# Kernel optimization log

Hardware: AMD Instinct MI355X
Metric: run time of the kernel (lower is better)

The kernel has to match this reference:

```python
import jax, jax.numpy as jnp
import numpy as np

HEADS = 8
DIM_HEAD = 64
NUM_MEM_KV = 4
DIM = 512
B, H, W = 16, 32, 32


def setup_inputs() -> dict:
    key = jax.random.key(0)
    k1, k2, k3, k4 = jax.random.split(key, 4)
    hidden = HEADS * DIM_HEAD
    x = jax.random.normal(k1, (B, DIM, H, W), dtype=jnp.float32)
    gamma = jnp.zeros((DIM,), dtype=jnp.float32)  # nn.Parameter init zeros
    mem_kv = jax.random.normal(k2, (2, HEADS, NUM_MEM_KV, DIM_HEAD), dtype=jnp.float32)
    w_qkv = jax.random.normal(k3, (3 * hidden, DIM), dtype=jnp.float32) * (1.0 / np.sqrt(DIM))
    w_out = jax.random.normal(k4, (DIM, hidden), dtype=jnp.float32) * (1.0 / np.sqrt(hidden))
    return {"x": x, "gamma": gamma, "mem_kv": mem_kv, "w_qkv": w_qkv, "w_out": w_out}


def reference(x, gamma, mem_kv, w_qkv, w_out):
    b, c, h, w = x.shape
    n = h * w
    # RMSNorm: F.normalize over channel dim, then * (gamma+1) * sqrt(dim)
    denom = jnp.maximum(jnp.linalg.norm(x, axis=1, keepdims=True), 1e-12)
    xn = (x / denom) * (gamma[None, :, None, None] + 1.0) * (c ** 0.5)
    # 1x1 conv qkv projection
    qkv = jnp.einsum('bchw,oc->bohw', xn, w_qkv)  # [b, 3*hidden, h, w]
    q, k, v = jnp.split(qkv, 3, axis=1)

    def to_heads(t):
        # 'b (h c) x y -> b h (x y) c'
        return t.reshape(b, HEADS, DIM_HEAD, n).transpose(0, 1, 3, 2)

    q = to_heads(q) * (DIM_HEAD ** -0.5)  # [b, heads, n, d]
    k = to_heads(k)
    v = to_heads(v)
    mk = jnp.broadcast_to(mem_kv[0], (b, HEADS, NUM_MEM_KV, DIM_HEAD))
    mv = jnp.broadcast_to(mem_kv[1], (b, HEADS, NUM_MEM_KV, DIM_HEAD))
    k = jnp.concatenate([mk, k], axis=2)  # [b, heads, m+n, d]
    v = jnp.concatenate([mv, v], axis=2)
    sim = jnp.einsum('bhid,bhjd->bhij', q, k)
    attn = jax.nn.softmax(sim, axis=-1)
    out = jnp.einsum('bhij,bhjd->bhid', attn, v)  # [b, heads, n, d]
    # 'b h (x y) d -> b (h d) x y'
    out = out.transpose(0, 1, 3, 2).reshape(b, HEADS * DIM_HEAD, h, w)
    return jnp.einsum('bchw,oc->bohw', out, w_out)
```

## Files before the change

kernel.cpp:

```cpp
#include <hip/hip_runtime.h>
#include <cstdint>
#include <cstddef>

constexpr int kHeads = 8;
constexpr int kDHead = 64;
constexpr int kC     = 512;
constexpr int kB     = 16;
constexpr int kN     = 1024;
constexpr int kHid   = 512;

typedef _Float16 h16;
typedef _Float16 h8 __attribute__((ext_vector_type(8)));
typedef _Float16 h4 __attribute__((ext_vector_type(4)));
typedef _Float16 h2 __attribute__((ext_vector_type(2)));
typedef float f32x4 __attribute__((ext_vector_type(4)));

__global__ __launch_bounds__(256) void rms_transpose_kernel(
    const float* __restrict__ x, h16* __restrict__ xh)
{
  __shared__ float T[64 * 64];
  __shared__ float red[4][64];
  __shared__ float sl[64];
  const int t  = threadIdx.x;
  const int b  = blockIdx.x >> 4;
  const int p0 = (blockIdx.x & 15) << 6;
  const float* xb = x + (size_t)b * kC * kN + p0;

  const int pix = t & 63, sub = t >> 6;
  float sum = 0.f;
  #pragma unroll 8
  for (int c = sub * 128; c < sub * 128 + 128; ++c) {
    const float v = xb[(size_t)c * kN + pix];
    sum = fmaf(v, v, sum);
  }
  red[sub][pix] = sum;
  __syncthreads();
  if (t < 64) {
    const float tot = red[0][t] + red[1][t] + red[2][t] + red[3][t];
    sl[t] = 22.62741699796952f / fmaxf(sqrtf(tot), 1e-12f);
  }
  __syncthreads();

  for (int cc = 0; cc < 8; cc++) {
    const int c0 = cc * 64;
    #pragma unroll
    for (int i = 0; i < 4; i++) {
      const int r  = i * 16 + (t >> 4);
      const int pg = t & 15;
      const float4 v = *(const float4*)(xb + (size_t)(c0 + r) * kN + pg * 4);
      *(float4*)&T[r * 64 + ((pg ^ (r & 15)) << 2)] = v;
    }
    __syncthreads();
    #pragma unroll
    for (int i2 = 0; i2 < 2; i2++) {
      const int p  = i2 * 32 + (t >> 3);
      const int cg = t & 7;
      const float sc = sl[p];
      h16 hv[8];
      #pragma unroll
      for (int j = 0; j < 8; j++) {
        const int c = cg * 8 + j;
        const float v = T[c * 64 + (((p >> 2) ^ (c & 15)) << 2) + (p & 3)];
        hv[j] = (h16)(v * sc);
      }
      *(h8*)&xh[((size_t)b * kN + p0 + p) * kC + c0 + cg * 8] = *(h8*)hv;
    }
    __syncthreads();
  }
}

__global__ __launch_bounds__(64) void prep_w_kernel(
    const float* __restrict__ w_qkv, const float* __restrict__ gamma,
    const float* __restrict__ w_out, h16* __restrict__ wqh,
    h16* __restrict__ wouth)
{
  const int row = blockIdx.x;
  const int c0  = threadIdx.x * 8;
  if (row < 1536) {
    const float sc = (row < 512) ? 0.125f * 1.4426950408889634f : 1.f;
    const float4 a  = *(const float4*)(w_qkv + (size_t)row * kC + c0);
    const float4 b  = *(const float4*)(w_qkv + (size_t)row * kC + c0 + 4);
    const float4 g0 = *(const float4*)(gamma + c0);
    const float4 g1 = *(const float4*)(gamma + c0 + 4);
    h8 hv = { (h16)(a.x * (g0.x + 1.f) * sc), (h16)(a.y * (g0.y + 1.f) * sc),
              (h16)(a.z * (g0.z + 1.f) * sc), (h16)(a.w * (g0.w + 1.f) * sc),
              (h16)(b.x * (g1.x + 1.f) * sc), (h16)(b.y * (g1.y + 1.f) * sc),
              (h16)(b.z * (g1.z + 1.f) * sc), (h16)(b.w * (g1.w + 1.f) * sc) };
    *(h8*)&wqh[(size_t)row * kC + c0] = hv;
  } else {
    const int r = row - 1536;
    const float4 a = *(const float4*)(w_out + (size_t)r * kC + c0);
    const float4 b = *(const float4*)(w_out + (size_t)r * kC + c0 + 4);
    h8 hv = { (h16)a.x, (h16)a.y, (h16)a.z, (h16)a.w,
              (h16)b.x, (h16)b.y, (h16)b.z, (h16)b.w };
    *(h8*)&wouth[(size_t)r * kC + c0] = hv;
  }
}

__device__ __forceinline__ void gemm_loop_f16(
    const h16* __restrict__ Ag, const h16* __restrict__ Bg,
    h16 (*__restrict__ As)[8192], h16 (*__restrict__ Bs)[8192],
    int t, int w, int g, int lo, f32x4 (&acc)[4][4])
{
  const int wo = (w >> 1) * 64, wp = (w & 1) * 64;
  h8 stA[4], stB[4];
  auto load = [&](int kt) {
    const int k0 = kt * 64;
    #pragma unroll
    for (int i = 0; i < 4; i++) {
      const int f = t + i * 256, r = f >> 3, cg = f & 7;
      stA[i] = *(const h8*)(Ag + (size_t)r * kC + k0 + cg * 8);
      stB[i] = *(const h8*)(Bg + (size_t)r * kC + k0 + cg * 8);
    }
  };
  auto store = [&](int buf) {
    #pragma unroll
    for (int i = 0; i < 4; i++) {
      const int f = t + i * 256, r = f >> 3, cg = f & 7;
      const int off = r * 64 + ((cg ^ (r & 7)) << 3);
      *(h8*)&As[buf][off] = stA[i];
      *(h8*)&Bs[buf][off] = stB[i];
    }
  };
  load(0); store(0); __syncthreads();
  int buf = 0;
  for (int kt = 0; kt < 8; kt++) {
    if (kt < 7) load(kt + 1);
    h8 bfr[4][2];
    #pragma unroll
    for (int ni = 0; ni < 4; ni++) {
      const int row = wp + ni * 16 + lo;
      #pragma unroll
      for (int kb = 0; kb < 2; kb++)
        bfr[ni][kb] = *(const h8*)&Bs[buf][row * 64 + (((kb * 4 + g) ^ (row & 7)) << 3)];
    }
    #pragma unroll
    for (int mi = 0; mi < 4; mi++) {
      const int row = wo + mi * 16 + lo;
      const h8 a0 = *(const h8*)&As[buf][row * 64 + (((    g) ^ (row & 7)) << 3)];
      const h8 a1 = *(const h8*)&As[buf][row * 64 + (((4 + g) ^ (row & 7)) << 3)];
      #pragma unroll
      for (int ni = 0; ni < 4; ni++) {
        acc[mi][ni] = __builtin_amdgcn_mfma_f32_16x16x32_f16(a0, bfr[ni][0], acc[mi][ni], 0, 0, 0);
        acc[mi][ni] = __builtin_amdgcn_mfma_f32_16x16x32_f16(a1, bfr[ni][1], acc[mi][ni], 0, 0, 0);
      }
    }
    if (kt < 7) store(buf ^ 1);
    __syncthreads();
    buf ^= 1;
  }
}

__global__ __launch_bounds__(256) void qkv_mfma_kernel(
    const h16* __restrict__ xh, const h16* __restrict__ wqh,
    h16* __restrict__ Qh, h16* __restrict__ Kh, h16* __restrict__ VTh)
{
  __shared__ h16 As[2][8192];
  __shared__ h16 Bs[2][8192];
  const int t = threadIdx.x, lane = t & 63, w = t >> 6, g = lane >> 4, lo = lane & 15;
  const int o0 = blockIdx.x * 128;
  const int p0 = blockIdx.y * 128;
  const int b  = blockIdx.z;
  const h16* Ag = wqh + (size_t)o0 * kC;
  const h16* Bg = xh + ((size_t)b * kN + p0) * kC;

  f32x4 acc[4][4];
  #pragma unroll
  for (int mi = 0; mi < 4; mi++)
    #pragma unroll
    for (int ni = 0; ni < 4; ni++) { f32x4 z = {0.f, 0.f, 0.f, 0.f}; acc[mi][ni] = z; }

  gemm_loop_f16(Ag, Bg, As, Bs, t, w, g, lo, acc);

  const int o_wave = o0 + (w >> 1) * 64;
  const int which  = o_wave >> 9;
  const int head   = (o_wave >> 6) & 7;
  const size_t bh  = (size_t)b * kHeads + head;
  const int pglob  = p0 + (w & 1) * 64;

  if (which == 2) {
    h16* Vdst = VTh + bh * (size_t)(kN * kDHead);
    #pragma unroll
    for (int mi = 0; mi < 4; mi++)
      #pragma unroll
      for (int ni = 0; ni < 4; ni++) {
        const int p = pglob + ni * 16 + lo;
        #pragma unroll
        for (int r = 0; r < 4; r++) {
          const int d = mi * 16 + g * 4 + r;
          Vdst[(size_t)d * kN + p] = (h16)((const float*)&acc[mi][ni])[r];
        }
      }
  } else {
    h16* lw = &As[0][0] + w * 4096;
    #pragma unroll
    for (int mi = 0; mi < 4; mi++) {
      const int gran0 = mi * 2 + (g >> 1);
      const int off   = (g & 1) * 4;
      #pragma unroll
      for (int ni = 0; ni < 4; ni++) {
        const int p = ni * 16 + lo;
        h4 pv = { (h16)acc[mi][ni].x, (h16)acc[mi][ni].y,
                  (h16)acc[mi][ni].z, (h16)acc[mi][ni].w };
        *(h4*)&lw[p * 64 + ((gran0 ^ (p & 7)) << 3) + off] = pv;
      }
    }
    __syncthreads();
    h16* dst = (which ? Kh : Qh) + bh * (size_t)(kN * kDHead);
    #pragma unroll
    for (int i = 0; i < 8; i++) {
      const int p  = i * 8 + (lane >> 3);
      const int dg = lane & 7;
      const h8 v = *(const h8*)&lw[p * 64 + ((dg ^ (p & 7)) << 3)];
      *(h8*)&dst[((size_t)pglob + p) * kDHead + dg * 8] = v;
    }
  }
}

__global__ __launch_bounds__(256, 3) void attn_mfma_kernel(
    const h16* __restrict__ Qh, const h16* __restrict__ Kh,
    const h16* __restrict__ VTh, const float* __restrict__ mem_kv,
    h16* __restrict__ ah)
{
  __shared__ h16 Kl[2][4096];
  __shared__ h16 Vl[2][4096];

  const int t    = threadIdx.x;
  const int lane = t & 63;
  const int w    = t >> 6;
  const int g    = lane >> 4;
  const int lo   = lane & 15;
  const int id   = blockIdx.x;
  const int xcd  = id & 7;
  const int slot = id >> 3;
  const int grp  = xcd * 16 + (slot & 15);
  const int qt   = slot >> 4;
  const int h = grp & 7, b = grp >> 3;
  const size_t bh = (size_t)b * kHeads + h;

  const h16* Qg = Qh  + bh * 65536;
  const h16* Kg = Kh  + bh * 65536;
  const h16* Vg = VTh + bh * 65536;
  const int q0 = qt * 128 + w * 32;

  h8 qf[2][2];
  #pragma unroll
  for (int ni = 0; ni < 2; ni++)
    #pragma unroll
    for (int kb = 0; kb < 2; kb++)
      qf[ni][kb] = *(const h8*)(Qg + (size_t)(q0 + ni*16 + lo) * 64 + kb*32 + g*8);

  {
    const int kr = t >> 2, dq = (t & 3) << 4;
    h16 hv[16];
    if (kr < 4) {
      const float* src = mem_kv + (size_t)h * 256 + kr * 64 + dq;
      #pragma unroll
      for (int i = 0; i < 16; i++) hv[i] = (h16)src[i];
    } else {
      #pragma unroll
      for (int i = 0; i < 16; i++) hv[i] = (h16)0.f;
    }
    const int sw = (kr & 7) << 3;
    *(h8*)&Kl[0][kr*64 + ( dq      ^ sw)] = *(h8*)&hv[0];
    *(h8*)&Kl[0][kr*64 + ((dq + 8) ^ sw)] = *(h8*)&hv[8];

    const int d = t >> 2, kq = (t & 3) << 4;
    h16 vv[16];
    #pragma unroll
    for (int i = 0; i < 16; i++) vv[i] = (h16)0.f;
    if (kq == 0) {
      const float* src = mem_kv + 2048 + (size_t)h * 256 + d;
      #pragma unroll
      for (int i = 0; i < 4; i++) vv[i] = (h16)src[i * 64];
    }
    const int sv = (d & 7) << 3;
    *(h8*)&Vl[0][d*64 + ( kq      ^ sv)] = *(h8*)&vv[0];
    *(h8*)&Vl[0][d*64 + ((kq + 8) ^ sv)] = *(h8*)&vv[8];
  }
  __syncthreads();

  f32x4 o[2][4];
  #pragma unroll
  for (int qb = 0; qb < 2; qb++)
    #pragma unroll
    for (int db = 0; db < 4; db++) { f32x4 z = {0.f,0.f,0.f,0.f}; o[qb][db] = z; }
  float lst[2] = {0.f, 0.f};

  h8 stK[2], stV[2];

  auto proc = [&](const h16* KL, const h16* VL, h16* KW, h16* VW,
                  int loadIdx, bool mask) {
    if (loadIdx < 16) {
      const size_t key0 = (size_t)loadIdx * 64;
      #pragma unroll
      for (int ps = 0; ps < 2; ps++) {
        const int f = t + ps*256, r = f >> 3, cb = (f & 7) << 3;
        stK[ps] = *(const h8*)(Kg + (key0 + r) * 64 + cb);
        stV[ps] = *(const h8*)(Vg + (size_t)r * 1024 + key0 + cb);
      }
    }

    f32x4 s[4][2];
    __builtin_amdgcn_s_setprio(1);
    #pragma unroll
    for (int mi = 0; mi < 4; mi++) {
      const int row = mi*16 + lo;
      const int sw = (row & 7) << 3;
      const h8 k0 = *(const h8*)&KL[row*64 + (( g*8)      ^ sw)];
      const h8 k1 = *(const h8*)&KL[row*64 + ((32 + g*8)  ^ sw)];
      float ci = -8.f;
      if (mask && (mi > 0 || g > 0)) ci = -1e30f;
      const f32x4 cinit = {ci, ci, ci, ci};
      #pragma unroll
      for (int ni = 0; ni < 2; ni++) {
        f32x4 acc = __builtin_amdgcn_mfma_f32_16x16x32_f16(k0, qf[ni][0], cinit, 0, 0, 0);
        acc = __builtin_amdgcn_mfma_f32_16x16x32_f16(k1, qf[ni][1], acc, 0, 0, 0);
        s[mi][ni] = acc;
      }
    }
    __builtin_amdgcn_s_setprio(0);

    h4 p4[4][2];
    #pragma unroll
    for (int ni = 0; ni < 2; ni++) {
      #pragma unroll
      for (int mi = 0; mi < 4; mi++) {
        const float px = exp2f(s[mi][ni].x);
        const float py = exp2f(s[mi][ni].y);
        const float pz = exp2f(s[mi][ni].z);
        const float pw = exp2f(s[mi][ni].w);
        lst[ni] += (px + py) + (pz + pw);
        const h2 a = __builtin_bit_cast(h2, __builtin_amdgcn_cvt_pkrtz(px, py));
        const h2 c = __builtin_bit_cast(h2, __builtin_amdgcn_cvt_pkrtz(pz, pw));
        p4[mi][ni] = __builtin_shufflevector(a, c, 0, 1, 2, 3);
      }
    }

    __builtin_amdgcn_s_setprio(1);
    #pragma unroll
    for (int db = 0; db < 4; db++) {
      const int d = db*16 + lo;
      const int sw = (d & 7) << 3;
      h4 v4[4];
      #pragma unroll
      for (int mi = 0; mi < 4; mi++)
        v4[mi] = *(const h4*)&VL[d*64 + ((mi*16 + (g>>1)*8) ^ sw) + (g&1)*4];
      #pragma unroll
      for (int qb = 0; qb < 2; qb++)
        #pragma unroll
        for (int mi = 0; mi < 4; mi++)
          o[qb][db] = __builtin_amdgcn_mfma_f32_16x16x16f16(p4[mi][qb], v4[mi], o[qb][db], 0, 0, 0);
    }
    __builtin_amdgcn_s_setprio(0);

    if (loadIdx < 16) {
      #pragma unroll
      for (int ps = 0; ps < 2; ps++) {
        const int f = t + ps*256, r = f >> 3, cb = (f & 7) << 3;
        const int sw = (r & 7) << 3;
        *(h8*)&KW[r*64 + (cb ^ sw)] = stK[ps];
        *(h8*)&VW[r*64 + (cb ^ sw)] = stV[ps];
      }
    }
    __syncthreads();
  };

  proc(Kl[0], Vl[0], Kl[1], Vl[1], 0, true);
  #pragma unroll 1
  for (int i = 0; i < 8; i++) {
    proc(Kl[1], Vl[1], Kl[0], Vl[0], 2*i + 1, false);
    proc(Kl[0], Vl[0], Kl[1], Vl[1], 2*i + 2, false);
  }

  #pragma unroll
  for (int qb = 0; qb < 2; qb++) {
    float l = lst[qb];
    l += __shfl_xor(l, 16);
    l += __shfl_xor(l, 32);
    const float il = 1.f / l;
    const float i0 = __shfl(il, g*4 + 0);
    const float i1 = __shfl(il, g*4 + 1);
    const float i2 = __shfl(il, g*4 + 2);
    const float i3 = __shfl(il, g*4 + 3);
    const int qg = (b << 10) + q0 + qb*16 + g*4;
    #pragma unroll
    for (int db = 0; db < 4; db++) {
      const int c = h*64 + db*16 + lo;
      ah[(size_t)(qg + 0) * kHid + c] = (h16)(o[qb][db].x * i0);
      ah[(size_t)(qg + 1) * kHid + c] = (h16)(o[qb][db].y * i1);
      ah[(size_t)(qg + 2) * kHid + c] = (h16)(o[qb][db].z * i2);
      ah[(size_t)(qg + 3) * kHid + c] = (h16)(o[qb][db].w * i3);
    }
  }
}

__global__ __launch_bounds__(256) void out_mfma_kernel(
    const h16* __restrict__ ah, const h16* __restrict__ wouth,
    float* __restrict__ out)
{
  __shared__ h16 As[2][8192];
  __shared__ h16 Bs[2][8192];
  const int t = threadIdx.x, lane = t & 63, w = t >> 6, g = lane >> 4, lo = lane & 15;
  const int o0 = blockIdx.x * 128;
  const int p0 = blockIdx.y * 128;
  const int b  = blockIdx.z;
  const h16* Ag = wouth + (size_t)o0 * kC;
  const h16* Bg = ah + ((size_t)b * kN + p0) * kC;

  f32x4 acc[4][4];
  #pragma unroll
  for (int mi = 0; mi < 4; mi++)
    #pragma unroll
    for (int ni = 0; ni < 4; ni++) { f32x4 z = {0.f, 0.f, 0.f, 0.f}; acc[mi][ni] = z; }

  gemm_loop_f16(Ag, Bg, As, Bs, t, w, g, lo, acc);

  const int ow = o0 + (w >> 1) * 64;
  const int pw = p0 + (w & 1) * 64;
  #pragma unroll
  for (int mi = 0; mi < 4; mi++)
    #pragma unroll
    for (int ni = 0; ni < 4; ni++) {
      const int p = pw + ni * 16 + lo;
      #pragma unroll
      for (int r = 0; r < 4; r++) {
        const int oc = ow + mi * 16 + g * 4 + r;
        out[((size_t)b * kHid + oc) * kN + p] = ((const float*)&acc[mi][ni])[r];
      }
    }
}

extern "C" void kernel_launch(void* const* d_in, const int* in_sizes, int n_in,
                              void* d_out, int out_size, void* d_ws, size_t ws_size,
                              hipStream_t stream) {
  (void)in_sizes; (void)n_in; (void)out_size; (void)ws_size;
  const float* x      = (const float*)d_in[0];
  const float* gamma  = (const float*)d_in[1];
  const float* mem_kv = (const float*)d_in[2];
  const float* w_qkv  = (const float*)d_in[3];
  const float* w_out  = (const float*)d_in[4];
  float* out = (float*)d_out;

  h16* xh    = (h16*)d_ws;
  h16* Qh    = xh + (size_t)16777216;
  h16* Kh    = Qh + (size_t)8388608;
  h16* VTh   = Kh + (size_t)8388608;
  h16* ah    = VTh + (size_t)8388608;
  h16* wqh   = ah + (size_t)8388608;
  h16* wouth = wqh + (size_t)786432;

  rms_transpose_kernel<<<256, 256, 0, stream>>>(x, xh);
  prep_w_kernel<<<2048, 64, 0, stream>>>(w_qkv, gamma, w_out, wqh, wouth);
  qkv_mfma_kernel<<<dim3(12, 8, 16), 256, 0, stream>>>(xh, wqh, Qh, Kh, VTh);
  attn_mfma_kernel<<<1024, 256, 0, stream>>>(Qh, Kh, VTh, mem_kv, ah);
  out_mfma_kernel<<<dim3(4, 8, 16), 256, 0, stream>>>(ah, wouth, out);
}
```

Baseline: 154.8 us.

## Use single-wave attention blocks reading K/V from global with prepended memory-KV tile

Memory K/V is written once by a new prep kernel as a padded 64-key tile at the front of enlarged K and V^T buffers, and the QKV GEMM writes after that tile. The attention kernel becomes one wave per block, 4096 blocks, and loads K and V fragments straight from global memory instead of staging them in double-buffered, swizzled LDS with barriers. The padded zero keys are no longer masked; their fixed exp2(-8) contribution is subtracted from the softmax denominator. This removes LDS traffic and barriers, but each wave now waits on uncoalesced global/L2 loads with no prefetch, and K/V is re-read once per wave rather than once per block.

```diff
diff --git a/kernel.cpp b/kernel.cpp
--- a/kernel.cpp
+++ b/kernel.cpp
@@ -8,6 +8,8 @@
 constexpr int kB     = 16;
 constexpr int kN     = 1024;
 constexpr int kHid   = 512;
+constexpr int kKeys  = 1088;
+constexpr int kKVsz  = kKeys * kDHead;
 
 typedef _Float16 h16;
 typedef _Float16 h8 __attribute__((ext_vector_type(8)));
@@ -97,6 +99,33 @@
   }
 }
 
+__global__ __launch_bounds__(64) void prep_memkv_kernel(
+    const float* __restrict__ mem_kv, h16* __restrict__ Kh2,
+    h16* __restrict__ VT2)
+{
+  const int bh = blockIdx.x;
+  const int h  = bh & 7;
+  const int t  = threadIdx.x;
+  h16* krow = Kh2 + (size_t)bh * kKVsz + t * kDHead;
+  if (t < 4) {
+    const float* src = mem_kv + (size_t)h * 256 + t * 64;
+    #pragma unroll
+    for (int j = 0; j < 64; j++) krow[j] = (h16)src[j];
+  } else {
+    #pragma unroll
+    for (int j = 0; j < 8; j++) *(h8*)&krow[j * 8] = (h8)0;
+  }
+  h16* vrow = VT2 + (size_t)bh * kKVsz + (size_t)t * kKeys;
+  h16 tmp[64];
+  #pragma unroll
+  for (int j = 0; j < 64; j++) tmp[j] = (h16)0.f;
+  #pragma unroll
+  for (int k = 0; k < 4; k++)
+    tmp[k] = (h16)mem_kv[2048 + (size_t)h * 256 + k * 64 + t];
+  #pragma unroll
+  for (int j = 0; j < 8; j++) *(h8*)&vrow[j * 8] = *(h8*)&tmp[j * 8];
+}
+
 __device__ __forceinline__ void gemm_loop_f16(
     const h16* __restrict__ Ag, const h16* __restrict__ Bg,
     h16 (*__restrict__ As)[8192], h16 (*__restrict__ Bs)[8192],
@@ -153,7 +182,7 @@
 
 __global__ __launch_bounds__(256) void qkv_mfma_kernel(
     const h16* __restrict__ xh, const h16* __restrict__ wqh,
-    h16* __restrict__ Qh, h16* __restrict__ Kh, h16* __restrict__ VTh)
+    h16* __restrict__ Qh, h16* __restrict__ Kh2, h16* __restrict__ VT2)
 {
   __shared__ h16 As[2][8192];
   __shared__ h16 Bs[2][8192];
@@ -179,7 +208,7 @@
   const int pglob  = p0 + (w & 1) * 64;
 
   if (which == 2) {
-    h16* Vdst = VTh + bh * (size_t)(kN * kDHead);
+    h16* Vdst = VT2 + bh * kKVsz;
     #pragma unroll
     for (int mi = 0; mi < 4; mi++)
       #pragma unroll
@@ -188,7 +217,7 @@
         #pragma unroll
         for (int r = 0; r < 4; r++) {
           const int d = mi * 16 + g * 4 + r;
-          Vdst[(size_t)d * kN + p] = (h16)((const float*)&acc[mi][ni])[r];
+          Vdst[(size_t)d * kKeys + 64 + p] = (h16)((const float*)&acc[mi][ni])[r];
         }
       }
   } else {
@@ -206,7 +235,7 @@
       }
     }
     __syncthreads();
-    h16* dst = (which ? Kh : Qh) + bh * (size_t)(kN * kDHead);
+    h16* dst = which ? (Kh2 + bh * kKVsz + 64 * kDHead) : (Qh + bh * (size_t)(kN * kDHead));
     #pragma unroll
     for (int i = 0; i < 8; i++) {
       const int p  = i * 8 + (lane >> 3);
@@ -217,31 +246,24 @@
   }
 }
 
-__global__ __launch_bounds__(256, 3) void attn_mfma_kernel(
-    const h16* __restrict__ Qh, const h16* __restrict__ Kh,
-    const h16* __restrict__ VTh, const float* __restrict__ mem_kv,
-    h16* __restrict__ ah)
-{
-  __shared__ h16 Kl[2][4096];
-  __shared__ h16 Vl[2][4096];
-
-  const int t    = threadIdx.x;
-  const int lane = t & 63;
-  const int w    = t >> 6;
-  const int g    = lane >> 4;
-  const int lo   = lane & 15;
+__global__ __launch_bounds__(64, 3) void attn_mfma_kernel(
+    const h16* __restrict__ Qh, const h16* __restrict__ Kh2,
+    const h16* __restrict__ VT2, h16* __restrict__ ah)
+{
+  const int lane = threadIdx.x;
+  const int g  = lane >> 4;
+  const int lo = lane & 15;
   const int id   = blockIdx.x;
   const int xcd  = id & 7;
   const int slot = id >> 3;
   const int grp  = xcd * 16 + (slot & 15);
   const int qt   = slot >> 4;
   const int h = grp & 7, b = grp >> 3;
-  const size_t bh = (size_t)b * kHeads + h;
-
-  const h16* Qg = Qh  + bh * 65536;
-  const h16* Kg = Kh  + bh * 65536;
-  const h16* Vg = VTh + bh * 65536;
-  const int q0 = qt * 128 + w * 32;
+  const int q0 = qt * 32;
+
+  const h16* Qg = Qh  + (size_t)grp * (kN * kDHead);
+  const h16* Kg = Kh2 + (size_t)grp * kKVsz;
+  const h16* Vg = VT2 + (size_t)grp * kKVsz;
 
   h8 qf[2][2];
   #pragma unroll
@@ -250,68 +272,25 @@
     for (int kb = 0; kb < 2; kb++)
       qf[ni][kb] = *(const h8*)(Qg + (size_t)(q0 + ni*16 + lo) * 64 + kb*32 + g*8);
 
-  {
-    const int kr = t >> 2, dq = (t & 3) << 4;
-    h16 hv[16];
-    if (kr < 4) {
-      const float* src = mem_kv + (size_t)h * 256 + kr * 64 + dq;
-      #pragma unroll
-      for (int i = 0; i < 16; i++) hv[i] = (h16)src[i];
-    } else {
-      #pragma unroll
-      for (int i = 0; i < 16; i++) hv[i] = (h16)0.f;
-    }
-    const int sw = (kr & 7) << 3;
-    *(h8*)&Kl[0][kr*64 + ( dq      ^ sw)] = *(h8*)&hv[0];
-    *(h8*)&Kl[0][kr*64 + ((dq + 8) ^ sw)] = *(h8*)&hv[8];
-
-    const int d = t >> 2, kq = (t & 3) << 4;
-    h16 vv[16];
-    #pragma unroll
-    for (int i = 0; i < 16; i++) vv[i] = (h16)0.f;
-    if (kq == 0) {
-      const float* src = mem_kv + 2048 + (size_t)h * 256 + d;
-      #pragma unroll
-      for (int i = 0; i < 4; i++) vv[i] = (h16)src[i * 64];
-    }
-    const int sv = (d & 7) << 3;
-    *(h8*)&Vl[0][d*64 + ( kq      ^ sv)] = *(h8*)&vv[0];
-    *(h8*)&Vl[0][d*64 + ((kq + 8) ^ sv)] = *(h8*)&vv[8];
-  }
-  __syncthreads();
-
   f32x4 o[2][4];
   #pragma unroll
   for (int qb = 0; qb < 2; qb++)
     #pragma unroll
     for (int db = 0; db < 4; db++) { f32x4 z = {0.f,0.f,0.f,0.f}; o[qb][db] = z; }
   float lst[2] = {0.f, 0.f};
-
-  h8 stK[2], stV[2];
-
-  auto proc = [&](const h16* KL, const h16* VL, h16* KW, h16* VW,
-                  int loadIdx, bool mask) {
-    if (loadIdx < 16) {
-      const size_t key0 = (size_t)loadIdx * 64;
-      #pragma unroll
-      for (int ps = 0; ps < 2; ps++) {
-        const int f = t + ps*256, r = f >> 3, cb = (f & 7) << 3;
-        stK[ps] = *(const h8*)(Kg + (key0 + r) * 64 + cb);
-        stV[ps] = *(const h8*)(Vg + (size_t)r * 1024 + key0 + cb);
-      }
-    }
+  const f32x4 cinit = {-8.f, -8.f, -8.f, -8.f};
+
+  for (int kt = 0; kt < 17; kt++) {
+    const h16* Kt = Kg + kt * (64 * kDHead);
+    const int key0 = kt * 64;
 
     f32x4 s[4][2];
     __builtin_amdgcn_s_setprio(1);
     #pragma unroll
     for (int mi = 0; mi < 4; mi++) {
       const int row = mi*16 + lo;
-      const int sw = (row & 7) << 3;
-      const h8 k0 = *(const h8*)&KL[row*64 + (( g*8)      ^ sw)];
-      const h8 k1 = *(const h8*)&KL[row*64 + ((32 + g*8)  ^ sw)];
-      float ci = -8.f;
-      if (mask && (mi > 0 || g > 0)) ci = -1e30f;
-      const f32x4 cinit = {ci, ci, ci, ci};
+      const h8 k0 = *(const h8*)(Kt + row*64      + g*8);
+      const h8 k1 = *(const h8*)(Kt + row*64 + 32 + g*8);
       #pragma unroll
       for (int ni = 0; ni < 2; ni++) {
         f32x4 acc = __builtin_amdgcn_mfma_f32_16x16x32_f16(k0, qf[ni][0], cinit, 0, 0, 0);
@@ -341,11 +320,10 @@
     #pragma unroll
     for (int db = 0; db < 4; db++) {
       const int d = db*16 + lo;
-      const int sw = (d & 7) << 3;
       h4 v4[4];
       #pragma unroll
       for (int mi = 0; mi < 4; mi++)
-        v4[mi] = *(const h4*)&VL[d*64 + ((mi*16 + (g>>1)*8) ^ sw) + (g&1)*4];
+        v4[mi] = *(const h4*)(Vg + (size_t)d * kKeys + key0 + mi*16 + g*4);
       #pragma unroll
       for (int qb = 0; qb < 2; qb++)
         #pragma unroll
@@ -353,24 +331,6 @@
           o[qb][db] = __builtin_amdgcn_mfma_f32_16x16x16f16(p4[mi][qb], v4[mi], o[qb][db], 0, 0, 0);
     }
     __builtin_amdgcn_s_setprio(0);
-
-    if (loadIdx < 16) {
-      #pragma unroll
-      for (int ps = 0; ps < 2; ps++) {
-        const int f = t + ps*256, r = f >> 3, cb = (f & 7) << 3;
-        const int sw = (r & 7) << 3;
-        *(h8*)&KW[r*64 + (cb ^ sw)] = stK[ps];
-        *(h8*)&VW[r*64 + (cb ^ sw)] = stV[ps];
-      }
-    }
-    __syncthreads();
-  };
-
-  proc(Kl[0], Vl[0], Kl[1], Vl[1], 0, true);
-  #pragma unroll 1
-  for (int i = 0; i < 8; i++) {
-    proc(Kl[1], Vl[1], Kl[0], Vl[0], 2*i + 1, false);
-    proc(Kl[0], Vl[0], Kl[1], Vl[1], 2*i + 2, false);
   }
 
   #pragma unroll
@@ -378,6 +338,7 @@
     float l = lst[qb];
     l += __shfl_xor(l, 16);
     l += __shfl_xor(l, 32);
+    l -= 0.234375f;
     const float il = 1.f / l;
     const float i0 = __shfl(il, g*4 + 0);
     const float i1 = __shfl(il, g*4 + 1);
@@ -443,16 +404,17 @@
   float* out = (float*)d_out;
 
   h16* xh    = (h16*)d_ws;
-  h16* Qh    = xh + (size_t)16777216;
-  h16* Kh    = Qh + (size_t)8388608;
-  h16* VTh   = Kh + (size_t)8388608;
-  h16* ah    = VTh + (size_t)8388608;
-  h16* wqh   = ah + (size_t)8388608;
-  h16* wouth = wqh + (size_t)786432;
+  h16* Qh    = xh   + (size_t)16777216;
+  h16* Kh2   = Qh   + (size_t)8388608;
+  h16* VT2   = Kh2  + (size_t)8912896;
+  h16* ah    = VT2  + (size_t)8912896;
+  h16* wqh   = ah   + (size_t)8388608;
+  h16* wouth = wqh  + (size_t)786432;
 
   rms_transpose_kernel<<<256, 256, 0, stream>>>(x, xh);
   prep_w_kernel<<<2048, 64, 0, stream>>>(w_qkv, gamma, w_out, wqh, wouth);
-  qkv_mfma_kernel<<<dim3(12, 8, 16), 256, 0, stream>>>(xh, wqh, Qh, Kh, VTh);
-  attn_mfma_kernel<<<1024, 256, 0, stream>>>(Qh, Kh, VTh, mem_kv, ah);
+  prep_memkv_kernel<<<128, 64, 0, stream>>>(mem_kv, Kh2, VT2);
+  qkv_mfma_kernel<<<dim3(12, 8, 16), 256, 0, stream>>>(xh, wqh, Qh, Kh2, VT2);
+  attn_mfma_kernel<<<4096, 64, 0, stream>>>(Qh, Kh2, VT2, ah);
   out_mfma_kernel<<<dim3(4, 8, 16), 256, 0, stream>>>(ah, wouth, out);
 }
```

Result: slower. 291.5 us (+88.2%).
